# Kernel tuning notes

Measured on AMD Instinct MI355X. Metric: run time of the kernel, lower is better.

## Reference

```python
import jax, jax.numpy as jnp
import numpy as np

DIM = 256
HEADS = 4
WIN = 128
PAD = (WIN - 1) // 2  # 63
SHIFT = WIN // 2      # 64
RED = 16              # SE reduction


def _hann(w):
    # torch.hann_window(w, periodic=False)
    n = jnp.arange(w, dtype=jnp.float32)
    return 0.5 * (1.0 - jnp.cos(2.0 * jnp.pi * n / (w - 1)))


def _layernorm(x, g, b, eps=1e-5):
    mu = jnp.mean(x, axis=-1, keepdims=True)
    var = jnp.var(x, axis=-1, keepdims=True)
    return (x - mu) * jax.lax.rsqrt(var + eps) * g + b


def _attend_windows(x, ln_g, ln_b, in_proj_w, in_proj_b, out_w, out_b):
    B, T, C = x.shape
    w = WIN
    h = HEADS
    d = C // h
    L = T + 2 * PAD - w + 1  # number of stride-1 windows (= T-1 for even w)
    y = _layernorm(x, ln_g, ln_b)
    y_pad = jnp.pad(y, ((0, 0), (PAD, PAD), (0, 0)))
    idx = jnp.arange(L)[:, None] + jnp.arange(w)[None, :]  # (L, w)
    win = y_pad[:, idx, :]  # (B, L, w, C) -- the unfold blowup
    win = win * _hann(w)[None, None, :, None]
    # fused qkv projection (torch MHA in_proj)
    qkv = jnp.einsum('blwc,ec->blwe', win, in_proj_w) + in_proj_b  # (B,L,w,3C)
    q, k, v = jnp.split(qkv, 3, axis=-1)
    q = q.reshape(B, L, w, h, d)
    k = k.reshape(B, L, w, h, d)
    v = v.reshape(B, L, w, h, d)
    scale = 1.0 / jnp.sqrt(jnp.asarray(d, dtype=x.dtype))
    scores = jnp.einsum('blqhd,blkhd->blhqk', q, k) * scale
    attn = jax.nn.softmax(scores, axis=-1)
    o = jnp.einsum('blhqk,blkhd->blqhd', attn, v).reshape(B, L, w, C)
    o = jnp.einsum('blwc,ec->blwe', o, out_w) + out_b  # out_proj
    # fold: overlap-add back to length T (crop padding)
    idx_flat = idx.reshape(-1)  # (L*w,)
    acc = jnp.zeros((B, T + 2 * PAD, C), dtype=x.dtype)
    acc = acc.at[:, idx_flat, :].add(o.reshape(B, L * w, C))
    y_out = acc[:, PAD:PAD + T, :]
    counts = jnp.zeros((T + 2 * PAD,), dtype=x.dtype).at[idx_flat].add(1.0)
    counts = counts[PAD:PAD + T]
    return y_out / (counts[None, :, None] + 1e-6)


def setup_inputs() -> dict:
    key = jax.random.key(0)
    ks = jax.random.split(key, 9)
    C = DIM
    s = 0.02
    return {
        'x': jax.random.normal(ks[0], (1, 1024, C), dtype=jnp.float32),
        'ln_g': jnp.ones((C,), jnp.float32),
        'ln_b': jnp.zeros((C,), jnp.float32),
        'in_proj_w': jax.random.normal(ks[1], (3 * C, C), jnp.float32) * s,
        'in_proj_b': jnp.zeros((3 * C,), jnp.float32),
        'out_w': jax.random.normal(ks[2], (C, C), jnp.float32) * s,
        'out_b': jnp.zeros((C,), jnp.float32),
        'proj_w': jax.random.normal(ks[3], (C, C), jnp.float32) * s,
        'proj_b': jnp.zeros((C,), jnp.float32),
        'se_w1': jax.random.normal(ks[4], (C // RED, C), jnp.float32) * s,
        'se_w2': jax.random.normal(ks[5], (C, C // RED), jnp.float32) * s,
    }


def reference(x, ln_g, ln_b, in_proj_w, in_proj_b, out_w, out_b, proj_w, proj_b, se_w1, se_w2):
    # T > window_size branch (1024 > 128)
    y_main = _attend_windows(x, ln_g, ln_b, in_proj_w, in_proj_b, out_w, out_b)
    x_shift = jnp.roll(x, SHIFT, axis=1)
    y_shift = _attend_windows(x_shift, ln_g, ln_b, in_proj_w, in_proj_b, out_w, out_b)
    y_shift = jnp.roll(y_shift, -SHIFT, axis=1)
    y = 0.5 * (y_main + y_shift)
    y = jnp.einsum('btc,ec->bte', y, proj_w) + proj_b  # proj (dropout p=0 -> identity)
    # SE module: global average over T, bottleneck MLP, sigmoid gate
    s = jnp.mean(y, axis=1)  # (B, C)
    s = jax.nn.relu(s @ se_w1.T)
    s = jax.nn.sigmoid(s @ se_w2.T)
    y = y * s[:, None, :]
    return x + y
```

## Files before the change

### kernel.cpp

```cpp
#include <hip/hip_runtime.h>

#define TLEN 1024
#define CDIM 256
#define NHEAD 4
#define HD 64
#define WIN_ 128
#define PADL 63
#define LWIN 1023
#define TPAD 1150
#define SW 32

typedef __attribute__((ext_vector_type(8))) short bf16x8;
typedef __attribute__((ext_vector_type(8))) _Float16 f16x8;
typedef __attribute__((ext_vector_type(2))) __fp16 fp16v2;
typedef __attribute__((ext_vector_type(4))) float f32x4;

__device__ __forceinline__ int prow(int v, int t) {
  if (v == 0) return t;
  if (t < PADL || t >= PADL + TLEN) return t;
  int s = t - PADL;
  s = (s + (TLEN - 64)) & (TLEN - 1);
  return PADL + s;
}

__device__ __forceinline__ float hannf(int j) {
  return 0.5f * (1.0f - __cosf(6.283185307179586f * (float)j / 127.0f));
}

__device__ __forceinline__ float countf(int t) {
  int lo = t - 127; if (lo < 0) lo = 0;
  int hi = t;       if (hi > LWIN - 1) hi = LWIN - 1;
  return (float)(hi - lo + 1);
}

__device__ __forceinline__ unsigned short bfr(float f) {
  unsigned int u = __float_as_uint(f);
  u += 0x7FFFu + ((u >> 16) & 1u);
  return (unsigned short)(u >> 16);
}
__device__ __forceinline__ unsigned int pk2t(float a, float b) {
  return __builtin_amdgcn_perm(__float_as_uint(b), __float_as_uint(a), 0x07060302u);
}
__device__ __forceinline__ float bfu(unsigned short u) {
  return __uint_as_float(((unsigned int)u) << 16);
}
__device__ __forceinline__ float bflo(unsigned int u) { return __uint_as_float(u << 16); }
__device__ __forceinline__ float bfhi(unsigned int u) { return __uint_as_float(u & 0xFFFF0000u); }

__device__ __forceinline__ float ex2(float x) {
  float r;
  asm("v_exp_f32 %0, %1" : "=v"(r) : "v"(x));
  return r;
}
__device__ __forceinline__ float rcpf(float x) {
  float r;
  asm("v_rcp_f32 %0, %1" : "=v"(r) : "v"(x));
  return r;
}

__device__ __forceinline__ unsigned int pkh(float lo, float hi) {
  union { fp16v2 h; unsigned int u; } c;
  c.h = __builtin_amdgcn_cvt_pkrtz(lo, hi);
  return c.u;
}
__device__ __forceinline__ unsigned short h16(float f) {
  union { _Float16 h; unsigned short u; } c;
  c.h = (_Float16)f;
  return c.u;
}
__device__ __forceinline__ unsigned int pkmul(unsigned int a, unsigned int b) {
  unsigned int r;
  asm("v_pk_mul_f16 %0, %1, %2" : "=v"(r) : "v"(a), "v"(b));
  return r;
}
__device__ __forceinline__ unsigned int exp2pk(unsigned int x) {
  unsigned int lo, hi;
  unsigned int xh = x >> 16;
  asm("v_exp_f16 %0, %1" : "=v"(lo) : "v"(x));
  asm("v_exp_f16 %0, %1" : "=v"(hi) : "v"(xh));
  return __builtin_amdgcn_perm(hi, lo, 0x05040100u);
}

#define AL16(h, l) ((((unsigned int)(l)) >> 16) | (((unsigned int)(h)) << 16))

#define QLOG2E 0.18033688011112042f

__global__ void k_prep(const float* __restrict__ x, const float* __restrict__ g,
                       const float* __restrict__ b, unsigned short* __restrict__ lnbf,
                       const float* __restrict__ W, unsigned short* __restrict__ Wb,
                       const float* __restrict__ pw, const float* __restrict__ ow,
                       const float* __restrict__ ob, unsigned short* __restrict__ Mtb,
                       float* __restrict__ vbv,
                       float* __restrict__ accg, unsigned short* __restrict__ Pbf,
                       float* __restrict__ msum) {
  __shared__ float pr[256];
  __shared__ float red[256];
  const int bid = blockIdx.x;
  const int tid = threadIdx.x;
  if (bid < 256) {
    int wv = tid >> 6, lane = tid & 63;
    int r = bid * 4 + wv;
    float4 v = ((const float4*)(x + (size_t)r * CDIM))[lane];
    float s = v.x + v.y + v.z + v.w;
    float q = v.x * v.x + v.y * v.y + v.z * v.z + v.w * v.w;
    #pragma unroll
    for (int m = 32; m >= 1; m >>= 1) { s += __shfl_xor(s, m); q += __shfl_xor(q, m); }
    float mu = s * (1.0f / 256.0f);
    float var = q * (1.0f / 256.0f) - mu * mu;
    float rs = rsqrtf(var + 1e-5f);
    float4 gg = ((const float4*)g)[lane];
    float4 bb = ((const float4*)b)[lane];
    uint2 o;
    o.x = (unsigned int)bfr((v.x - mu) * rs * gg.x + bb.x) |
          ((unsigned int)bfr((v.y - mu) * rs * gg.y + bb.y) << 16);
    o.y = (unsigned int)bfr((v.z - mu) * rs * gg.z + bb.z) |
          ((unsigned int)bfr((v.w - mu) * rs * gg.w + bb.w) << 16);
    ((uint2*)(lnbf + (size_t)r * CDIM))[lane] = o;
  } else if (bid < 352) {
    int i = (bid - 256) * 256 + tid;
    const float4* src = (const float4*)W;
    float4 a = src[2 * i], c = src[2 * i + 1];
    uint4 o;
    o.x = (unsigned int)bfr(a.x) | ((unsigned int)bfr(a.y) << 16);
    o.y = (unsigned int)bfr(a.z) | ((unsigned int)bfr(a.w) << 16);
    o.z = (unsigned int)bfr(c.x) | ((unsigned int)bfr(c.y) << 16);
    o.w = (unsigned int)bfr(c.z) | ((unsigned int)bfr(c.w) << 16);
    ((uint4*)Wb)[i] = o;
  } else if (bid < 608) {
    const int e = bid - 352;
    pr[tid] = pw[(size_t)e * CDIM + tid];
    __syncthreads();
    float a0 = 0.f, a1 = 0.f, a2 = 0.f, a3 = 0.f;
    for (int m = 0; m < 256; m += 4) {
      a0 += pr[m] * ow[(size_t)m * CDIM + tid];
      a1 += pr[m + 1] * ow[(size_t)(m + 1) * CDIM + tid];
      a2 += pr[m + 2] * ow[(size_t)(m + 2) * CDIM + tid];
      a3 += pr[m + 3] * ow[(size_t)(m + 3) * CDIM + tid];
    }
    Mtb[(size_t)e * CDIM + tid] = bfr((a0 + a1) + (a2 + a3));
    red[tid] = pr[tid] * ob[tid];
    __syncthreads();
    for (int s = 128; s > 0; s >>= 1) { if (tid < s) red[tid] += red[tid + s]; __syncthreads(); }
    if (tid == 0) vbv[e] = red[0];
  } else if (bid < 624) {
    uint4 zz = make_uint4(0, 0, 0, 0);
    for (int i = (bid - 608) * 256 + tid; i < 147200; i += 16 * 256)
      ((uint4*)accg)[i] = zz;
  } else {
    uint4 zz = make_uint4(0, 0, 0, 0);
    for (int i = (bid - 624) * 256 + tid; i < 12096; i += 16 * 256) {
      int idx = (i < 6048) ? i : (104352 + (i - 6048));
      ((uint4*)Pbf)[idx] = zz;
    }
    if (bid == 624 && tid < 64) ((float4*)msum)[tid] = make_float4(0.f, 0.f, 0.f, 0.f);
  }
}

__launch_bounds__(512, 1)
__global__ void k_proj(const unsigned short* __restrict__ lnbf,
                       const unsigned short* __restrict__ Wb,
                       unsigned short* __restrict__ Pbf) {
  __shared__ __align__(16) unsigned short Ps[32 * 128];
  const int tid = threadIdx.x;
  const int lane = tid & 63, wv = tid >> 6;
  const int li16 = lane & 15, q4 = lane >> 4;
  const int ws = wv & 1, we = wv >> 1;
  const int sbase = blockIdx.x * 32;
  const int ebase = blockIdx.y * 128;
  const int s0 = sbase + ws * 16;
  const int e0 = ebase + we * 32;

  f32x4 acc[2];
  acc[0] = (f32x4){0.f, 0.f, 0.f, 0.f};
  acc[1] = (f32x4){0.f, 0.f, 0.f, 0.f};

  #pragma unroll
  for (int ks = 0; ks < 8; ++ks) {
    bf16x8 Af = *(const bf16x8*)(lnbf + (size_t)(s0 + li16) * 256 + ks * 32 + q4 * 8);
    #pragma unroll
    for (int et = 0; et < 2; ++et) {
      bf16x8 Bf = *(const bf16x8*)(Wb + (size_t)(e0 + 16 * et + li16) * 256 + ks * 32 + q4 * 8);
      acc[et] = __builtin_amdgcn_mfma_f32_16x16x32_bf16(Af, Bf, acc[et], 0, 0, 0);
    }
  }
  #pragma unroll
  for (int et = 0; et < 2; ++et)
    #pragma unroll
    for (int r = 0; r < 4; ++r) {
      int lr = ws * 16 + 4 * q4 + r;
      int lc = we * 32 + 16 * et + li16;
      Ps[lr * 128 + lc] = bfr(acc[et][r]);
    }
  __syncthreads();
  {
    int r = tid >> 4, c = (tid & 15) * 8;
    *(uint4*)(Pbf + (size_t)(PADL + sbase + r) * 768 + ebase + c) = *(uint4*)&Ps[r * 128 + c];
  }
}

__device__ __forceinline__ void stage_load(const unsigned short* __restrict__ Pbf,
                                           int v, int hd, int l0, int w, int stid,
                                           uint4& A, uint4& B) {
  const int jp = stid & 63;
  const int dg = stid >> 6;
  const int j0 = 2 * jp;
  int row0 = prow(v, l0 + w + j0);
  int row1 = prow(v, l0 + w + j0 + 1);
  A = *(const uint4*)(Pbf + (size_t)row0 * 768 + 512 + hd * 64 + dg * 8);
  B = *(const uint4*)(Pbf + (size_t)row1 * 768 + 512 + hd * 64 + dg * 8);
}

__device__ __forceinline__ void stage_write(unsigned short* vt, int w, int stid,
                                            const float* __restrict__ bB,
                                            const float* __restrict__ hth,
                                            uint4 a, uint4 b) {
  const int jp = stid & 63;
  const int dg = stid >> 6;
  const int j0 = 2 * jp;
  const int p0 = w + j0;
  float h0 = hth[j0], h1 = hth[j0 + 1];
  float e0 = ex2(h0 * bB[p0]);
  float e1 = ex2(h1 * bB[p0 + 1]);
  float f0 = e0 * h0, f1 = e1 * h1;
  unsigned int av[4] = {a.x, a.y, a.z, a.w};
  unsigned int bv[4] = {b.x, b.y, b.z, b.w};
  #pragma unroll
  for (int q = 0; q < 4; ++q) {
    int d0 = dg * 8 + 2 * q;
    unsigned int w0 = pkh(f0 * bflo(av[q]), f1 * bflo(bv[q]));
    unsigned int w1 = pkh(f0 * bfhi(av[q]), f1 * bfhi(bv[q]));
    *(unsigned int*)&vt[d0 * 128 + (j0 ^ ((d0 & 7) << 3))] = w0;
    *(unsigned int*)&vt[(d0 + 1) * 128 + (j0 ^ (((d0 + 1) & 7) << 3))] = w1;
  }
  if (stid < 64) {
    *(unsigned int*)&vt[64 * 128 + j0] = pkh(e0, e1);
  }
}

__launch_bounds__(1024, 4)
__global__ void k_attn(const unsigned short* __restrict__ Pbf, const float* __restrict__ ipb,
                       float* __restrict__ accg) {
  __shared__ __align__(16) unsigned short band[160 * 168];
  __shared__ __align__(16) unsigned short Vt[2][80 * 128];
  __shared__ __align__(16) unsigned char uni[159 * 68 * 4];
  __shared__ float hth[128];
  __shared__ float bB[160];
  __shared__ float bqS[64];

  unsigned short* Pq = (unsigned short*)uni;
  unsigned short* Pk = Pq + 159 * 64;
  float* accs = (float*)uni;

  const int strip = blockIdx.x, hd = blockIdx.y, v = blockIdx.z;
  const int l0 = strip * SW;
  const int nw = (SW < LWIN - l0) ? SW : (LWIN - l0);
  const int span = nw - 1 + WIN_;
  const int tid = threadIdx.x;
  const int lane = tid & 63;
  const int wv16 = tid >> 6;
  const int wg = wv16 >> 3;
  const int wv = wv16 & 7;
  const int stid = tid & 511;
  const int li16 = lane & 15, q4 = lane >> 4;
  const int iw = 16 * wv + li16;

  uint4 sA, sB;
  stage_load(Pbf, v, hd, l0, wg, stid, sA, sB);

  if (tid < 128) hth[tid] = hannf(tid);
  if (tid < 64) bqS[tid] = ipb[hd * 64 + tid];
  for (int i = tid; i < span * 8; i += 1024) {
    int t = i >> 3, dg = i & 7;
    int row = prow(v, l0 + t);
    const unsigned short* src = Pbf + (size_t)row * 768 + hd * 64;
    uint4 q = *(const uint4*)(src + dg * 8);
    uint4 k = *(const uint4*)(src + 256 + dg * 8);
    int off = (dg * 8) ^ ((t & 7) << 3);
    *(uint4*)&Pq[t * 64 + off] = q;
    *(uint4*)&Pk[t * 64 + off] = k;
  }
  {
    uint4 zz = make_uint4(0, 0, 0, 0);
    for (int i = tid; i < 480; i += 1024) {
      int bidx = i / 240, k = i % 240;
      *(uint4*)&Vt[bidx][65 * 128 + k * 8] = zz;
    }
  }
  __syncthreads();

  for (int p = tid; p < span; p += 1024) {
    float b = 0.0f;
    int sw = (p & 7) << 3;
    for (int d = 0; d < 64; ++d) b += bqS[d] * bfu(Pk[p * 64 + (d ^ sw)]);
    bB[p] = b * QLOG2E;
  }
  for (int tile = wv16; tile < 100; tile += 16) {
    int ta = tile / 10, tb = tile - 10 * (tile / 10);
    int tqa = 16 * ta + li16, swq = (tqa & 7) << 3;
    bf16x8 Aq0 = *(bf16x8*)&Pq[tqa * 64 + ((8 * q4) ^ swq)];
    bf16x8 Aq1 = *(bf16x8*)&Pq[tqa * 64 + ((32 + 8 * q4) ^ swq)];
    int tkb = 16 * tb + li16, swk = (tkb & 7) << 3;
    bf16x8 Bk0 = *(bf16x8*)&Pk[tkb * 64 + ((8 * q4) ^ swk)];
    bf16x8 Bk1 = *(bf16x8*)&Pk[tkb * 64 + ((32 + 8 * q4) ^ swk)];
    f32x4 D = (f32x4){0.f, 0.f, 0.f, 0.f};
    D = __builtin_amdgcn_mfma_f32_16x16x32_bf16(Aq0, Bk0, D, 0, 0, 0);
    D = __builtin_amdgcn_mfma_f32_16x16x32_bf16(Aq1, Bk1, D, 0, 0, 0);
    #pragma unroll
    for (int r = 0; r < 4; ++r)
      band[(16 * ta + 4 * q4 + r) * 168 + 16 * tb + li16] = h16(D[r]);
  }
  __syncthreads();

  for (int i = tid; i < 159 * 68; i += 1024) accs[i] = 0.0f;
  if (wg == 0) stage_write(&Vt[0][0], 0, stid, bB, hth, sA, sB);
  else         stage_write(&Vt[1][0], 1, stid, bB, hth, sA, sB);
  __syncthreads();

  unsigned int hh2p[16];
  {
    const float h_i = hth[iw];
    #pragma unroll
    for (int ks = 0; ks < 4; ++ks)
      #pragma unroll
      for (int q = 0; q < 4; ++q) {
        float lo = h_i * hth[32 * ks + 8 * q4 + 2 * q] * QLOG2E;
        float hi = h_i * hth[32 * ks + 8 * q4 + 2 * q + 1] * QLOG2E;
        hh2p[ks * 4 + q] = pkh(lo, hi);
      }
  }

  #pragma unroll 1
  for (int wp = 0; wp < nw; wp += 2) {
    const int w = wp + wg;
    const bool act = (w < nw);
    const int wnext = wp + 2 + wg;
    if (wnext < nw) stage_load(Pbf, v, hd, l0, wnext, stid, sA, sB);

    f32x4 O[5];
    #pragma unroll
    for (int mt = 0; mt < 5; ++mt) O[mt] = (f32x4){0.f, 0.f, 0.f, 0.f};

    if (act) {
      const int m = w & 7;
      const unsigned short* brow = &band[(w + iw) * 168 + (w & ~7)];
      const unsigned short* vt = &Vt[wg][0];

      #pragma unroll
      for (int ks = 0; ks < 4; ++ks) {
        uint4 R0 = *(const uint4*)&brow[32 * ks + 8 * q4];
        uint4 R1 = *(const uint4*)&brow[32 * ks + 8 * q4 + 8];
        unsigned int d0 = R0.x, d1 = R0.y, d2 = R0.z, d3 = R0.w;
        unsigned int d4 = R1.x, d5 = R1.y, d6 = R1.z, d7 = R1.w;
        unsigned int o0, o1, o2, o3;
        switch (m) {
          case 0: o0 = d0; o1 = d1; o2 = d2; o3 = d3; break;
          case 1: o0 = AL16(d1, d0); o1 = AL16(d2, d1); o2 = AL16(d3, d2); o3 = AL16(d4, d3); break;
          case 2: o0 = d1; o1 = d2; o2 = d3; o3 = d4; break;
          case 3: o0 = AL16(d2, d1); o1 = AL16(d3, d2); o2 = AL16(d4, d3); o3 = AL16(d5, d4); break;
          case 4: o0 = d2; o1 = d3; o2 = d4; o3 = d5; break;
          case 5: o0 = AL16(d3, d2); o1 = AL16(d4, d3); o2 = AL16(d5, d4); o3 = AL16(d6, d5); break;
          case 6: o0 = d3; o1 = d4; o2 = d5; o3 = d6; break;
          default: o0 = AL16(d4, d3); o1 = AL16(d5, d4); o2 = AL16(d6, d5); o3 = AL16(d7, d6); break;
        }
        unsigned int m0 = pkmul(hh2p[ks * 4 + 0], o0);
        unsigned int m1 = pkmul(hh2p[ks * 4 + 1], o1);
        unsigned int m2 = pkmul(hh2p[ks * 4 + 2], o2);
        unsigned int m3 = pkmul(hh2p[ks * 4 + 3], o3);
        union { uint4 u; f16x8 f; } cvt;
        cvt.u.x = exp2pk(m0);
        cvt.u.y = exp2pk(m1);
        cvt.u.z = exp2pk(m2);
        cvt.u.w = exp2pk(m3);
        f16x8 Bf = cvt.f;

        #pragma unroll
        for (int mt = 0; mt < 5; ++mt) {
          int d = 16 * mt + li16;
          f16x8 Af = *(const f16x8*)&vt[d * 128 + ((32 * ks + 8 * q4) ^ ((d & 7) << 3))];
          O[mt] = __builtin_amdgcn_mfma_f32_16x16x32_f16(Af, Bf, O[mt], 0, 0, 0);
        }
      }
    }

    if (wg == 0) {
      float nn = __shfl(O[4][0], li16);
      float sc = rcpf(nn);
      float* arow = &accs[(w + iw) * 68];
      #pragma unroll
      for (int mt = 0; mt < 4; ++mt) {
        int c = 16 * mt + 4 * q4;
        float4 cur = *(float4*)&arow[c];
        cur.x += O[mt][0] * sc; cur.y += O[mt][1] * sc;
        cur.z += O[mt][2] * sc; cur.w += O[mt][3] * sc;
        *(float4*)&arow[c] = cur;
      }
    }
    __syncthreads();

    if (wg == 1 && act) {
      float nn = __shfl(O[4][0], li16);
      float sc = rcpf(nn);
      float* arow = &accs[(w + iw) * 68];
      #pragma unroll
      for (int mt = 0; mt < 4; ++mt) {
        int c = 16 * mt + 4 * q4;
        float4 cur = *(float4*)&arow[c];
        cur.x += O[mt][0] * sc; cur.y += O[mt][1] * sc;
        cur.z += O[mt][2] * sc; cur.w += O[mt][3] * sc;
        *(float4*)&arow[c] = cur;
      }
    }
    if (wnext < nw) stage_write(&Vt[wg][0], wnext, stid, bB, hth, sA, sB);
    __syncthreads();
  }

  float* av = accg + (size_t)v * TPAD * CDIM;
  for (int i = tid; i < span * 64; i += 1024) {
    int p = i >> 6, dd = i & 63;
    int lo = p - 127; if (lo < 0) lo = 0;
    int hi = p; if (hi > nw - 1) hi = nw - 1;
    float cnt = (float)(hi - lo + 1);
    float bvd = ipb[512 + hd * 64 + dd];
    atomicAdd(&av[(size_t)(l0 + p) * CDIM + hd * 64 + dd],
              accs[p * 68 + dd] + cnt * bvd);
  }
}

__launch_bounds__(512, 2)
__global__ void k_comb(const float* __restrict__ accg, const unsigned short* __restrict__ Mtb,
                       const float* __restrict__ vbv, const float* __restrict__ pb,
                       float* __restrict__ z, float* __restrict__ msum) {
  __shared__ __align__(16) unsigned short Ub[32 * 264];
  __shared__ float cfA[32], cfB[32], bscL[32];
  __shared__ float msB[128];
  const int tid = threadIdx.x;
  const int lane = tid & 63, wv = tid >> 6;
  const int li16 = lane & 15, q4 = lane >> 4;
  const int t0 = blockIdx.x * 32;
  const int e0 = blockIdx.y * 128;

  if (tid < 32) {
    int s = t0 + tid;
    float c0 = countf(PADL + s);
    float c1 = countf(PADL + ((s + 64) & (TLEN - 1)));
    float fA = 0.5f / (c0 + 1e-6f), fB = 0.5f / (c1 + 1e-6f);
    cfA[tid] = fA; cfB[tid] = fB;
    bscL[tid] = c0 * fA + c1 * fB;
  }
  if (tid < 128) msB[tid] = 0.0f;
  __syncthreads();

  for (int i = tid; i < 32 * 128; i += 512) {
    int rr = i >> 7, c2 = (i & 127) * 2;
    int s = t0 + rr;
    int s1 = (s + 64) & (TLEN - 1);
    float2 a0 = *(const float2*)&accg[(size_t)(PADL + s) * CDIM + c2];
    float2 a1 = *(const float2*)&accg[(size_t)TPAD * CDIM + (size_t)(PADL + s1) * CDIM + c2];
    float fA = cfA[rr], fB = cfB[rr];
    *(unsigned int*)&Ub[rr * 264 + c2] =
        pk2t(a0.x * fA + a1.x * fB, a0.y * fA + a1.y * fB);
  }
  __syncthreads();

  f32x4 acc[2];
  acc[0] = (f32x4){0.f, 0.f, 0.f, 0.f};
  acc[1] = (f32x4){0.f, 0.f, 0.f, 0.f};
  #pragma unroll
  for (int ks = 0; ks < 8; ++ks) {
    bf16x8 Bf = *(const bf16x8*)(Mtb + (size_t)(e0 + wv * 16 + li16) * 256 + ks * 32 + q4 * 8);
    #pragma unroll
    for (int it = 0; it < 2; ++it) {
      bf16x8 Af = *(bf16x8*)&Ub[(16 * it + li16) * 264 + ks * 32 + q4 * 8];
      acc[it] = __builtin_amdgcn_mfma_f32_16x16x32_bf16(Af, Bf, acc[it], 0, 0, 0);
    }
  }

  {
    int e = e0 + wv * 16 + li16;
    float vbe = vbv[e], pbe = pb[e];
    float part = 0.0f;
    #pragma unroll
    for (int it = 0; it < 2; ++it)
      #pragma unroll
      for (int r = 0; r < 4; ++r) {
        int rloc = 16 * it + 4 * q4 + r;
        float val = acc[it][r] + bscL[rloc] * vbe + pbe;
        z[(size_t)(t0 + rloc) * CDIM + e] = val;
        part += val;
      }
    atomicAdd(&msB[e - e0], part);
  }
  __syncthreads();
  if (tid < 128) atomicAdd(&msum[e0 + tid], msB[tid]);
}

__global__ void k_finalse(const float* __restrict__ x, const float* __restrict__ z,
                          const float* __restrict__ msum, const float* __restrict__ w1,
                          const float* __restrict__ w2, float* __restrict__ out) {
  __shared__ float red2[16][4];
  __shared__ float s1[16];
  __shared__ float gateS[256];
  int tid = threadIdx.x;
  int lane = tid & 63, wv = tid >> 6;
  float sm = msum[tid] * (1.0f / 1024.0f);
  #pragma unroll
  for (int r = 0; r < 16; ++r) {
    float v = sm * w1[(size_t)r * 256 + tid];
    #pragma unroll
    for (int m = 32; m >= 1; m >>= 1) v += __shfl_xor(v, m);
    if (lane == 0) red2[r][wv] = v;
  }
  __syncthreads();
  if (tid < 16) {
    float a = red2[tid][0] + red2[tid][1] + red2[tid][2] + red2[tid][3];
    s1[tid] = fmaxf(a, 0.0f);
  }
  __syncthreads();
  float gacc = 0.0f;
  #pragma unroll
  for (int i = 0; i < 16; ++i) gacc += s1[i] * w2[(size_t)tid * 16 + i];
  gateS[tid] = 1.0f / (1.0f + __expf(-gacc));
  __syncthreads();
  int i = blockIdx.x * 256 + tid;
  float4 xv = ((const float4*)x)[i];
  float4 zv = ((const float4*)z)[i];
  float4 gv = ((const float4*)gateS)[i & 63];
  float4 o;
  o.x = xv.x + zv.x * gv.x;
  o.y = xv.y + zv.y * gv.y;
  o.z = xv.z + zv.z * gv.z;
  o.w = xv.w + zv.w * gv.w;
  ((float4*)out)[i] = o;
}

extern "C" void kernel_launch(void* const* d_in, const int* in_sizes, int n_in,
                              void* d_out, int out_size, void* d_ws, size_t ws_size,
                              hipStream_t stream) {
  const float* x   = (const float*)d_in[0];
  const float* lng = (const float*)d_in[1];
  const float* lnb = (const float*)d_in[2];
  const float* ipw = (const float*)d_in[3];
  const float* ipb = (const float*)d_in[4];
  const float* ow  = (const float*)d_in[5];
  const float* ob  = (const float*)d_in[6];
  const float* pw  = (const float*)d_in[7];
  const float* pb  = (const float*)d_in[8];
  const float* w1  = (const float*)d_in[9];
  const float* w2  = (const float*)d_in[10];
  float* out = (float*)d_out;

  float* ws = (float*)d_ws;
  unsigned short* lnbf = (unsigned short*)ws;
  unsigned short* Wb   = (unsigned short*)(ws + 131072);
  unsigned short* Pbf  = (unsigned short*)(ws + 229376);
  float* accg = ws + 229376 + 441600;
  unsigned short* Mtb = (unsigned short*)(accg + 588800);
  float* vbv  = accg + 588800 + 32768;
  float* z    = vbv + 256;
  float* msum = z + 262144;

  k_prep<<<dim3(640), dim3(256), 0, stream>>>(x, lng, lnb, lnbf, ipw, Wb,
                                              pw, ow, ob, Mtb, vbv, accg, Pbf, msum);
  k_proj<<<dim3(32, 6), dim3(512), 0, stream>>>(lnbf, Wb, Pbf);
  k_attn<<<dim3(32, NHEAD, 2), dim3(1024), 0, stream>>>(Pbf, ipb, accg);
  k_comb<<<dim3(32, 2), dim3(512), 0, stream>>>(accg, Mtb, vbv, pb, z, msum);
  k_finalse<<<dim3(256), dim3(256), 0, stream>>>(x, z, msum, w1, w2, out);
}
```

Measured before the change: 171.3 us.

## Halve row tiles in proj/comb kernels, add MFMA priority, shuffle-reduce in prep

k_proj and k_comb now use 16-row tiles instead of 32, doubling the grid (64x6 and 64x2 blocks) so the small GEMMs spread across more compute units. In the attention kernel, wave priority is raised around the PV MFMA loop. The block reduction in k_prep is replaced with wavefront shuffles plus a 4-entry shared combine. The cost is more blocks, each doing less work, and weights reloaded per block.

```diff
diff --git a/kernel.cpp b/kernel.cpp
--- a/kernel.cpp
+++ b/kernel.cpp
@@ -94,7 +94,7 @@
                        float* __restrict__ accg, unsigned short* __restrict__ Pbf,
                        float* __restrict__ msum) {
   __shared__ float pr[256];
-  __shared__ float red[256];
+  __shared__ float red[4];
   const int bid = blockIdx.x;
   const int tid = threadIdx.x;
   if (bid < 256) {
@@ -138,10 +138,12 @@
       a3 += pr[m + 3] * ow[(size_t)(m + 3) * CDIM + tid];
     }
     Mtb[(size_t)e * CDIM + tid] = bfr((a0 + a1) + (a2 + a3));
-    red[tid] = pr[tid] * ob[tid];
+    float rv = pr[tid] * ob[tid];
+    #pragma unroll
+    for (int m = 32; m >= 1; m >>= 1) rv += __shfl_xor(rv, m);
+    if ((tid & 63) == 0) red[tid >> 6] = rv;
     __syncthreads();
-    for (int s = 128; s > 0; s >>= 1) { if (tid < s) red[tid] += red[tid + s]; __syncthreads(); }
-    if (tid == 0) vbv[e] = red[0];
+    if (tid == 0) vbv[e] = (red[0] + red[1]) + (red[2] + red[3]);
   } else if (bid < 624) {
     uint4 zz = make_uint4(0, 0, 0, 0);
     for (int i = (bid - 608) * 256 + tid; i < 147200; i += 16 * 256)
@@ -160,39 +162,26 @@
 __global__ void k_proj(const unsigned short* __restrict__ lnbf,
                        const unsigned short* __restrict__ Wb,
                        unsigned short* __restrict__ Pbf) {
-  __shared__ __align__(16) unsigned short Ps[32 * 128];
+  __shared__ __align__(16) unsigned short Ps[16 * 128];
   const int tid = threadIdx.x;
   const int lane = tid & 63, wv = tid >> 6;
   const int li16 = lane & 15, q4 = lane >> 4;
-  const int ws = wv & 1, we = wv >> 1;
-  const int sbase = blockIdx.x * 32;
+  const int sbase = blockIdx.x * 16;
   const int ebase = blockIdx.y * 128;
-  const int s0 = sbase + ws * 16;
-  const int e0 = ebase + we * 32;
-
-  f32x4 acc[2];
-  acc[0] = (f32x4){0.f, 0.f, 0.f, 0.f};
-  acc[1] = (f32x4){0.f, 0.f, 0.f, 0.f};
-
+  const int e0 = ebase + wv * 16;
+
+  f32x4 acc = (f32x4){0.f, 0.f, 0.f, 0.f};
   #pragma unroll
   for (int ks = 0; ks < 8; ++ks) {
-    bf16x8 Af = *(const bf16x8*)(lnbf + (size_t)(s0 + li16) * 256 + ks * 32 + q4 * 8);
-    #pragma unroll
-    for (int et = 0; et < 2; ++et) {
-      bf16x8 Bf = *(const bf16x8*)(Wb + (size_t)(e0 + 16 * et + li16) * 256 + ks * 32 + q4 * 8);
-      acc[et] = __builtin_amdgcn_mfma_f32_16x16x32_bf16(Af, Bf, acc[et], 0, 0, 0);
-    }
+    bf16x8 Af = *(const bf16x8*)(lnbf + (size_t)(sbase + li16) * 256 + ks * 32 + q4 * 8);
+    bf16x8 Bf = *(const bf16x8*)(Wb + (size_t)(e0 + li16) * 256 + ks * 32 + q4 * 8);
+    acc = __builtin_amdgcn_mfma_f32_16x16x32_bf16(Af, Bf, acc, 0, 0, 0);
   }
   #pragma unroll
-  for (int et = 0; et < 2; ++et)
-    #pragma unroll
-    for (int r = 0; r < 4; ++r) {
-      int lr = ws * 16 + 4 * q4 + r;
-      int lc = we * 32 + 16 * et + li16;
-      Ps[lr * 128 + lc] = bfr(acc[et][r]);
-    }
-  __syncthreads();
-  {
+  for (int r = 0; r < 4; ++r)
+    Ps[(4 * q4 + r) * 128 + wv * 16 + li16] = bfr(acc[r]);
+  __syncthreads();
+  if (tid < 256) {
     int r = tid >> 4, c = (tid & 15) * 8;
     *(uint4*)(Pbf + (size_t)(PADL + sbase + r) * 768 + ebase + c) = *(uint4*)&Ps[r * 128 + c];
   }
@@ -373,12 +362,14 @@
         cvt.u.w = exp2pk(m3);
         f16x8 Bf = cvt.f;
 
+        __builtin_amdgcn_s_setprio(1);
         #pragma unroll
         for (int mt = 0; mt < 5; ++mt) {
           int d = 16 * mt + li16;
           f16x8 Af = *(const f16x8*)&vt[d * 128 + ((32 * ks + 8 * q4) ^ ((d & 7) << 3))];
           O[mt] = __builtin_amdgcn_mfma_f32_16x16x32_f16(Af, Bf, O[mt], 0, 0, 0);
         }
+        __builtin_amdgcn_s_setprio(0);
       }
     }
 
@@ -430,16 +421,16 @@
 __global__ void k_comb(const float* __restrict__ accg, const unsigned short* __restrict__ Mtb,
                        const float* __restrict__ vbv, const float* __restrict__ pb,
                        float* __restrict__ z, float* __restrict__ msum) {
-  __shared__ __align__(16) unsigned short Ub[32 * 264];
-  __shared__ float cfA[32], cfB[32], bscL[32];
+  __shared__ __align__(16) unsigned short Ub[16 * 264];
+  __shared__ float cfA[16], cfB[16], bscL[16];
   __shared__ float msB[128];
   const int tid = threadIdx.x;
   const int lane = tid & 63, wv = tid >> 6;
   const int li16 = lane & 15, q4 = lane >> 4;
-  const int t0 = blockIdx.x * 32;
+  const int t0 = blockIdx.x * 16;
   const int e0 = blockIdx.y * 128;
 
-  if (tid < 32) {
+  if (tid < 16) {
     int s = t0 + tid;
     float c0 = countf(PADL + s);
     float c1 = countf(PADL + ((s + 64) & (TLEN - 1)));
@@ -450,7 +441,7 @@
   if (tid < 128) msB[tid] = 0.0f;
   __syncthreads();
 
-  for (int i = tid; i < 32 * 128; i += 512) {
+  for (int i = tid; i < 16 * 128; i += 512) {
     int rr = i >> 7, c2 = (i & 127) * 2;
     int s = t0 + rr;
     int s1 = (s + 64) & (TLEN - 1);
@@ -462,17 +453,12 @@
   }
   __syncthreads();
 
-  f32x4 acc[2];
-  acc[0] = (f32x4){0.f, 0.f, 0.f, 0.f};
-  acc[1] = (f32x4){0.f, 0.f, 0.f, 0.f};
+  f32x4 acc = (f32x4){0.f, 0.f, 0.f, 0.f};
   #pragma unroll
   for (int ks = 0; ks < 8; ++ks) {
     bf16x8 Bf = *(const bf16x8*)(Mtb + (size_t)(e0 + wv * 16 + li16) * 256 + ks * 32 + q4 * 8);
-    #pragma unroll
-    for (int it = 0; it < 2; ++it) {
-      bf16x8 Af = *(bf16x8*)&Ub[(16 * it + li16) * 264 + ks * 32 + q4 * 8];
-      acc[it] = __builtin_amdgcn_mfma_f32_16x16x32_bf16(Af, Bf, acc[it], 0, 0, 0);
-    }
+    bf16x8 Af = *(bf16x8*)&Ub[li16 * 264 + ks * 32 + q4 * 8];
+    acc = __builtin_amdgcn_mfma_f32_16x16x32_bf16(Af, Bf, acc, 0, 0, 0);
   }
 
   {
@@ -480,14 +466,12 @@
     float vbe = vbv[e], pbe = pb[e];
     float part = 0.0f;
     #pragma unroll
-    for (int it = 0; it < 2; ++it)
-      #pragma unroll
-      for (int r = 0; r < 4; ++r) {
-        int rloc = 16 * it + 4 * q4 + r;
-        float val = acc[it][r] + bscL[rloc] * vbe + pbe;
-        z[(size_t)(t0 + rloc) * CDIM + e] = val;
-        part += val;
-      }
+    for (int r = 0; r < 4; ++r) {
+      int rloc = 4 * q4 + r;
+      float val = acc[r] + bscL[rloc] * vbe + pbe;
+      z[(size_t)(t0 + rloc) * CDIM + e] = val;
+      part += val;
+    }
     atomicAdd(&msB[e - e0], part);
   }
   __syncthreads();
@@ -561,8 +545,8 @@
 
   k_prep<<<dim3(640), dim3(256), 0, stream>>>(x, lng, lnb, lnbf, ipw, Wb,
                                               pw, ow, ob, Mtb, vbv, accg, Pbf, msum);
-  k_proj<<<dim3(32, 6), dim3(512), 0, stream>>>(lnbf, Wb, Pbf);
+  k_proj<<<dim3(64, 6), dim3(512), 0, stream>>>(lnbf, Wb, Pbf);
   k_attn<<<dim3(32, NHEAD, 2), dim3(1024), 0, stream>>>(Pbf, ipb, accg);
-  k_comb<<<dim3(32, 2), dim3(512), 0, stream>>>(accg, Mtb, vbv, pb, z, msum);
+  k_comb<<<dim3(64, 2), dim3(512), 0, stream>>>(accg, Mtb, vbv, pb, z, msum);
   k_finalse<<<dim3(256), dim3(256), 0, stream>>>(x, z, msum, w1, w2, out);
 }
```

New measurement: 172.0 us. About the same (+0.5%).
